# Kernel tuning notes

Measured on AMD Instinct MI355X. Metric: run time of the kernel, lower is better.

## Reference

```python
import jax, jax.numpy as jnp
import numpy as np

N, E = 50000, 800000
F_IN, F_OUT, H, F_EDGE = 256, 32, 8, 5
LEAKY_SLOPE = 0.2


def setup_inputs() -> dict:
    key = jax.random.key(0)
    ks = jax.random.split(key, 6)
    x = jax.random.normal(ks[0], (N, F_IN), dtype=jnp.float32)
    edge_index = jax.random.randint(ks[1], (2, E), 0, N, dtype=jnp.int64)
    edge_attr = jax.random.normal(ks[2], (E, F_EDGE), dtype=jnp.float32)
    degree_src = jax.random.randint(ks[3], (E,), 0, 64, dtype=jnp.int64)
    # Xavier-uniform params
    lim_W = float(np.sqrt(6.0 / (F_IN + F_OUT)))
    W = jax.random.uniform(ks[4], (H, F_IN, F_OUT), minval=-lim_W, maxval=lim_W, dtype=jnp.float32)
    A = 2 * F_OUT + F_EDGE
    lim_a = float(np.sqrt(6.0 / (H + A)))
    a = jax.random.uniform(ks[5], (H, A), minval=-lim_a, maxval=lim_a, dtype=jnp.float32)
    lim_e = float(np.sqrt(1.0 / F_EDGE))
    W_edge_w = jax.random.uniform(jax.random.fold_in(key, 7), (F_EDGE, F_EDGE), minval=-lim_e, maxval=lim_e, dtype=jnp.float32)
    return {"x": x, "edge_index": edge_index, "edge_attr": edge_attr,
            "degree_src": degree_src, "W": W, "a": a, "W_edge_w": W_edge_w}


def reference(x, edge_index, edge_attr, degree_src, W, a, W_edge_w):
    n = x.shape[0]
    h, f_out = W.shape[0], W.shape[2]
    src, dst = edge_index[0], edge_index[1]
    # per-head projection: (N, H, F_out)
    Wh = jnp.einsum('nf,hfo->nho', x, W)
    # split attention vector instead of materializing the concat
    a_src, a_dst, a_e = a[:, :f_out], a[:, f_out:2 * f_out], a[:, 2 * f_out:]
    ef = edge_attr @ W_edge_w.T                      # (E, F_edge)
    e = (jnp.einsum('eho,ho->eh', Wh[src], a_src)
         + jnp.einsum('eho,ho->eh', Wh[dst], a_dst)
         + ef @ a_e.T)                                # (E, H)
    e = jax.nn.leaky_relu(e, LEAKY_SLOPE)
    scale = 1.0 / jnp.sqrt(jnp.clip(degree_src.astype(jnp.float32), 1.0, None))
    e = e * scale[:, None]
    # segment softmax over src; torch scatter_reduce amax include_self=True with zeros init -> max includes 0
    e_max = jnp.maximum(jax.ops.segment_max(e, src, num_segments=n), 0.0)
    e_exp = jnp.exp(e - e_max[src])
    e_sum = jax.ops.segment_sum(e_exp, src, num_segments=n)
    alpha = e_exp / (e_sum[src] + 1e-16)             # (E, H)
    msg = Wh[dst] * alpha[:, :, None]                # (E, H, F_out)
    out = jax.ops.segment_sum(msg, src, num_segments=n)
    out = jax.nn.elu(out.reshape(n, h * f_out))
    return out, alpha
```

## Files before the change

### kernel.cpp

```cpp
#include <hip/hip_runtime.h>
#include <hip/hip_bf16.h>
#include <math.h>

#define NN 50000
#define NE 800000
#define FIN 256
#define FOUT 32
#define NH 8
#define FE 5
#define AROW 69
#define NROWS_PAD 50048
#define BSTRIDE 48

typedef float f32x4 __attribute__((ext_vector_type(4)));
typedef short bf16x8 __attribute__((ext_vector_type(8)));

static __device__ __forceinline__ unsigned short f2bf(float f) {
    unsigned u = __float_as_uint(f);
    unsigned r = (u + 0x7FFFu + ((u >> 16) & 1u)) >> 16;
    return (unsigned short)r;
}
static __device__ __forceinline__ float bf2f(unsigned short b) {
    return __uint_as_float(((unsigned)b) << 16);
}
static __device__ __forceinline__ short f2bf_fast(float f) {
    __hip_bfloat16 h = __float2bfloat16(f);
    return *reinterpret_cast<short*>(&h);
}

__global__ __launch_bounds__(256) void k_prepre(const float* __restrict__ W,
                                                const float* __restrict__ a,
                                                const float* __restrict__ Wew,
                                                const int* __restrict__ ei,
                                                float* __restrict__ C,
                                                unsigned short* __restrict__ Bh,
                                                unsigned short* __restrict__ Bsh,
                                                unsigned short* __restrict__ Bsl,
                                                int* __restrict__ counts,
                                                int* __restrict__ pos) {
    int b = blockIdx.x, t = threadIdx.x;
    int i = b * 256 + t;
    if (i < NE / 4) {
        int4 e4 = *(const int4*)&ei[i * 4];
        int4 pv;
        pv.x = atomicAdd(&counts[e4.x], 1);
        pv.y = atomicAdd(&counts[e4.y], 1);
        pv.z = atomicAdd(&counts[e4.z], 1);
        pv.w = atomicAdd(&counts[e4.w], 1);
        *(int4*)&pos[i * 4] = pv;
    }
    if (b < 256) {
        int c = b, k = t;
        int h = c >> 5, o = c & 31;
        Bh[c * 256 + k] = f2bf(W[(size_t)h * (FIN * FOUT) + (size_t)k * FOUT + o]);
    } else if (b == 256) {
        if (t < NH * FE) {
            int h = t / FE, k = t % FE;
            float s = 0.f;
            for (int j = 0; j < FE; ++j) s += a[h * AROW + 2 * FOUT + j] * Wew[j * FE + k];
            C[t] = s;
        }
        int k = t;
        for (int h = 0; h < NH; ++h) {
            float s1v = 0.f, s2v = 0.f;
            for (int o = 0; o < FOUT; ++o) {
                float wv = W[(size_t)h * (FIN * FOUT) + (size_t)k * FOUT + o];
                s1v += wv * a[h * AROW + o];
                s2v += wv * a[h * AROW + FOUT + o];
            }
            unsigned short h1 = f2bf(s1v);
            Bsh[h * 256 + k] = h1;
            Bsl[h * 256 + k] = f2bf(s1v - bf2f(h1));
            unsigned short h2 = f2bf(s2v);
            Bsh[(8 + h) * 256 + k] = h2;
            Bsl[(8 + h) * 256 + k] = f2bf(s2v - bf2f(h2));
        }
    }
}

__global__ __launch_bounds__(256) void k_gemm_mfma(const float* __restrict__ x,
                                                   const unsigned short* __restrict__ Bh,
                                                   const unsigned short* __restrict__ Bsh,
                                                   const unsigned short* __restrict__ Bsl,
                                                   unsigned short* __restrict__ Whb,
                                                   float* __restrict__ s1,
                                                   float* __restrict__ s2, int nrows) {
    int t = threadIdx.x;
    int w = t >> 6, l = t & 63;
    int r = l & 15, blk = l >> 4;
    int row0 = blockIdx.x * 32;
    int c0 = w * 64;

    f32x4 acc[2][4];
    f32x4 acc_s = (f32x4)(0.f);
#pragma unroll
    for (int i = 0; i < 2; ++i)
#pragma unroll
        for (int j = 0; j < 4; ++j) acc[i][j] = (f32x4)(0.f);

    const float* ap[2];
#pragma unroll
    for (int rt = 0; rt < 2; ++rt) {
        int row = row0 + rt * 16 + r;
        if (row >= nrows) row = nrows - 1;
        ap[rt] = x + (size_t)row * 256 + blk * 8;
    }

#pragma unroll
    for (int ks = 0; ks < 8; ++ks) {
        const int k0 = ks * 32;
        bf16x8 ah[2];
#pragma unroll
        for (int rt = 0; rt < 2; ++rt) {
            f32x4 u0 = *(const f32x4*)(ap[rt] + k0);
            f32x4 u1 = *(const f32x4*)(ap[rt] + k0 + 4);
            ah[rt][0] = f2bf_fast(u0.x); ah[rt][1] = f2bf_fast(u0.y);
            ah[rt][2] = f2bf_fast(u0.z); ah[rt][3] = f2bf_fast(u0.w);
            ah[rt][4] = f2bf_fast(u1.x); ah[rt][5] = f2bf_fast(u1.y);
            ah[rt][6] = f2bf_fast(u1.z); ah[rt][7] = f2bf_fast(u1.w);
        }
        bf16x8 bh[4];
#pragma unroll
        for (int ct = 0; ct < 4; ++ct) {
            int c = c0 + ct * 16 + r;
            bh[ct] = *(const bf16x8*)&Bh[c * 256 + k0 + blk * 8];
        }
#pragma unroll
        for (int ct = 0; ct < 4; ++ct) {
#pragma unroll
            for (int rt = 0; rt < 2; ++rt)
                acc[rt][ct] = __builtin_amdgcn_mfma_f32_16x16x32_bf16(ah[rt], bh[ct], acc[rt][ct], 0, 0, 0);
        }
        if (w < 2) {
            bf16x8 bsh = *(const bf16x8*)&Bsh[r * 256 + k0 + blk * 8];
            bf16x8 bsl = *(const bf16x8*)&Bsl[r * 256 + k0 + blk * 8];
            acc_s = __builtin_amdgcn_mfma_f32_16x16x32_bf16(ah[w], bsh, acc_s, 0, 0, 0);
            acc_s = __builtin_amdgcn_mfma_f32_16x16x32_bf16(ah[w], bsl, acc_s, 0, 0, 0);
        }
    }

#pragma unroll
    for (int rt = 0; rt < 2; ++rt) {
#pragma unroll
        for (int reg = 0; reg < 4; ++reg) {
            int row = row0 + rt * 16 + blk * 4 + reg;
            if (row < nrows) {
#pragma unroll
                for (int ct = 0; ct < 4; ++ct)
                    Whb[(size_t)row * 256 + c0 + ct * 16 + r] = f2bf(acc[rt][ct][reg]);
            }
        }
    }
    if (w < 2) {
#pragma unroll
        for (int reg = 0; reg < 4; ++reg) {
            int row = row0 + w * 16 + blk * 4 + reg;
            if (row < nrows) {
                if (r < 8) s1[row * NH + r] = acc_s[reg];
                else       s2[row * NH + (r - 8)] = acc_s[reg];
            }
        }
    }
}

__global__ __launch_bounds__(256) void k_scatlog(const int* __restrict__ ei,
                                                 const float* __restrict__ eattr,
                                                 const int* __restrict__ degs,
                                                 const float* __restrict__ s1,
                                                 const float* __restrict__ s2,
                                                 const float* __restrict__ C,
                                                 const int* __restrict__ pos,
                                                 unsigned short* __restrict__ e_perm,
                                                 int2* __restrict__ de_perm) {
    __shared__ float Cl[NH * FE];
    int t = threadIdx.x;
    if (t < NH * FE) Cl[t] = C[t];
    __syncthreads();
    int e = blockIdx.x * 256 + t;
    if (e >= NE) return;
    int src = ei[e], dst = ei[NE + e];
    int dg = degs[e];
    float scale = rsqrtf((float)(dg > 1 ? dg : 1));
    float ea0 = eattr[(size_t)e * FE + 0];
    float ea1 = eattr[(size_t)e * FE + 1];
    float ea2 = eattr[(size_t)e * FE + 2];
    float ea3 = eattr[(size_t)e * FE + 3];
    float ea4 = eattr[(size_t)e * FE + 4];
    float4 s1a = *(const float4*)&s1[src * NH];
    float4 s1b = *(const float4*)&s1[src * NH + 4];
    float4 s2a = *(const float4*)&s2[dst * NH];
    float4 s2b = *(const float4*)&s2[dst * NH + 4];
    float vs1[8] = {s1a.x, s1a.y, s1a.z, s1a.w, s1b.x, s1b.y, s1b.z, s1b.w};
    float vs2[8] = {s2a.x, s2a.y, s2a.z, s2a.w, s2b.x, s2b.y, s2b.z, s2b.w};
    bf16x8 v;
#pragma unroll
    for (int h = 0; h < NH; ++h) {
        float q = vs1[h] + vs2[h] + ea0 * Cl[h * FE + 0] + ea1 * Cl[h * FE + 1] +
                  ea2 * Cl[h * FE + 2] + ea3 * Cl[h * FE + 3] + ea4 * Cl[h * FE + 4];
        q = q > 0.f ? q : 0.2f * q;
        v[h] = (short)f2bf(q * scale);
    }
    int ps = pos[e];
    if (ps < BSTRIDE) {
        int p = src * BSTRIDE + ps;
        *(bf16x8*)&e_perm[(size_t)p * 8] = v;
        de_perm[p] = make_int2(dst, e);
    }
}

__global__ __launch_bounds__(256) void k_smmsg(const int* __restrict__ counts,
                                               const unsigned short* __restrict__ e_perm,
                                               const int2* __restrict__ de_perm,
                                               const unsigned short* __restrict__ Whb,
                                               float* __restrict__ out_alpha,
                                               float* __restrict__ out) {
    __shared__ float al[4][256];
    __shared__ int dl[4][32];
    __shared__ int el[4][32];
    int t = threadIdx.x;
    int w = t >> 6, l = t & 63;
    int n = blockIdx.x * 4 + w;
    if (n >= NN) return;
    int start = n * BSTRIDE;
    int deg = counts[n];
    if (deg > BSTRIDE) deg = BSTRIDE;
    int j = l >> 3, h = l & 7;

    float vc[4];
#pragma unroll
    for (int q = 0; q < 4; ++q) {
        int b = j + 8 * q;
        vc[q] = (b < deg) ? bf2f(e_perm[(size_t)(start + b) * 8 + h]) : -1e30f;
    }
    float mx = 0.f;
#pragma unroll
    for (int q = 0; q < 4; ++q) mx = fmaxf(mx, vc[q]);
    for (int b = 32 + j; b < deg; b += 8)
        mx = fmaxf(mx, bf2f(e_perm[(size_t)(start + b) * 8 + h]));
    mx = fmaxf(mx, __shfl_xor(mx, 8));
    mx = fmaxf(mx, __shfl_xor(mx, 16));
    mx = fmaxf(mx, __shfl_xor(mx, 32));
    float m = mx;
    float ex[4];
    float sm = 0.f;
#pragma unroll
    for (int q = 0; q < 4; ++q) { ex[q] = __expf(vc[q] - m); sm += ex[q]; }
    for (int b = 32 + j; b < deg; b += 8)
        sm += __expf(bf2f(e_perm[(size_t)(start + b) * 8 + h]) - m);
    sm += __shfl_xor(sm, 8);
    sm += __shfl_xor(sm, 16);
    sm += __shfl_xor(sm, 32);
    float inv = 1.f / (sm + 1e-16f);
    f32x4 acc = (f32x4)(0.f);
    int hh = l >> 3;
    for (int base = 0; base < deg; base += 32) {
        int cnt = deg - base;
        if (cnt > 32) cnt = 32;
        if (l < cnt) {
            int2 de = de_perm[start + base + l];
            dl[w][l] = de.x;
            el[w][l] = de.y;
        }
        asm volatile("s_waitcnt lgkmcnt(0)" ::: "memory");
#pragma unroll
        for (int q = 0; q < 4; ++q) {
            int b = base + j + 8 * q;
            if (b < deg) {
                float av = (base == 0 ? ex[q]
                                      : __expf(bf2f(e_perm[(size_t)(start + b) * 8 + h]) - m)) * inv;
                al[w][(j + 8 * q) * 8 + h] = av;
                out_alpha[(size_t)el[w][j + 8 * q] * 8 + h] = av;
            }
        }
        asm volatile("s_waitcnt lgkmcnt(0)" ::: "memory");
        int jj = 0;
        for (; jj + 4 <= cnt; jj += 4) {
            int d0 = dl[w][jj], d1 = dl[w][jj + 1], d2 = dl[w][jj + 2], d3 = dl[w][jj + 3];
            float a0 = al[w][jj * 8 + hh],      a1 = al[w][jj * 8 + 8 + hh];
            float a2 = al[w][jj * 8 + 16 + hh], a3 = al[w][jj * 8 + 24 + hh];
            ushort4 u0 = *(const ushort4*)&Whb[(size_t)d0 * 256 + l * 4];
            ushort4 u1 = *(const ushort4*)&Whb[(size_t)d1 * 256 + l * 4];
            ushort4 u2 = *(const ushort4*)&Whb[(size_t)d2 * 256 + l * 4];
            ushort4 u3 = *(const ushort4*)&Whb[(size_t)d3 * 256 + l * 4];
            acc.x += a0 * bf2f(u0.x) + a1 * bf2f(u1.x) + a2 * bf2f(u2.x) + a3 * bf2f(u3.x);
            acc.y += a0 * bf2f(u0.y) + a1 * bf2f(u1.y) + a2 * bf2f(u2.y) + a3 * bf2f(u3.y);
            acc.z += a0 * bf2f(u0.z) + a1 * bf2f(u1.z) + a2 * bf2f(u2.z) + a3 * bf2f(u3.z);
            acc.w += a0 * bf2f(u0.w) + a1 * bf2f(u1.w) + a2 * bf2f(u2.w) + a3 * bf2f(u3.w);
        }
        for (; jj < cnt; ++jj) {
            int d0 = dl[w][jj];
            float a0 = al[w][jj * 8 + hh];
            ushort4 u0 = *(const ushort4*)&Whb[(size_t)d0 * 256 + l * 4];
            acc.x += a0 * bf2f(u0.x);
            acc.y += a0 * bf2f(u0.y);
            acc.z += a0 * bf2f(u0.z);
            acc.w += a0 * bf2f(u0.w);
        }
        asm volatile("s_waitcnt lgkmcnt(0)" ::: "memory");
    }
    f32x4 o;
    o.x = acc.x > 0.f ? acc.x : expm1f(acc.x);
    o.y = acc.y > 0.f ? acc.y : expm1f(acc.y);
    o.z = acc.z > 0.f ? acc.z : expm1f(acc.z);
    o.w = acc.w > 0.f ? acc.w : expm1f(acc.w);
    *(f32x4*)&out[(size_t)n * 256 + l * 4] = o;
}

extern "C" void kernel_launch(void* const* d_in, const int* in_sizes, int n_in,
                              void* d_out, int out_size, void* d_ws, size_t ws_size,
                              hipStream_t stream) {
    const float* x     = (const float*)d_in[0];
    const int*   ei    = (const int*)d_in[1];
    const float* eattr = (const float*)d_in[2];
    const int*   degs  = (const int*)d_in[3];
    const float* W     = (const float*)d_in[4];
    const float* a     = (const float*)d_in[5];
    const float* Wew   = (const float*)d_in[6];

    float* out       = (float*)d_out;
    float* out_alpha = out + (size_t)NN * 256;

    char* p = (char*)d_ws;
    auto alloc = [&](size_t bytes) -> char* {
        char* r = p;
        p += (bytes + 255) & ~(size_t)255;
        return r;
    };
    unsigned short* Whb     = (unsigned short*)alloc((size_t)NN * 256 * 2);
    float*          s1      = (float*)alloc((size_t)NN * NH * 4);
    float*          s2      = (float*)alloc((size_t)NN * NH * 4);
    float*          Cm      = (float*)alloc(NH * FE * 4);
    unsigned short* Bh      = (unsigned short*)alloc((size_t)256 * 256 * 2);
    unsigned short* Bsh     = (unsigned short*)alloc((size_t)16 * 256 * 2);
    unsigned short* Bsl     = (unsigned short*)alloc((size_t)16 * 256 * 2);
    int*            counts  = (int*)alloc((size_t)NN * 4);
    int*            pos     = (int*)alloc((size_t)NE * 4);
    unsigned short* e_perm  = (unsigned short*)alloc(((size_t)NN * BSTRIDE + 64) * NH * 2);
    int2*           de_perm = (int2*)alloc(((size_t)NN * BSTRIDE + 64) * 8);

    hipMemsetAsync(counts, 0, (size_t)NN * 4, stream);

    k_prepre<<<(NE / 4 + 255) / 256, 256, 0, stream>>>(W, a, Wew, ei, Cm, Bh,
                                                       Bsh, Bsl, counts, pos);
    k_gemm_mfma<<<NROWS_PAD / 32, 256, 0, stream>>>(x, Bh, Bsh, Bsl, Whb, s1, s2, NN);
    k_scatlog<<<(NE + 255) / 256, 256, 0, stream>>>(ei, eattr, degs, s1, s2, Cm,
                                                    pos, e_perm, de_perm);
    k_smmsg<<<(NN + 3) / 4, 256, 0, stream>>>(counts, e_perm, de_perm, Whb,
                                              out_alpha, out);
}
```

Measured before the change: 223.1 us.

## Stage bf16 A tile in LDS and double GEMM row tile to 64

```diff
diff --git a/kernel.cpp b/kernel.cpp
--- a/kernel.cpp
+++ b/kernel.cpp
@@ -11,6 +11,7 @@
 #define AROW 69
 #define NROWS_PAD 50048
 #define BSTRIDE 48
+#define ASTRIDE 264
 
 typedef float f32x4 __attribute__((ext_vector_type(4)));
 typedef short bf16x8 __attribute__((ext_vector_type(8)));
@@ -85,53 +86,58 @@
                                                    unsigned short* __restrict__ Whb,
                                                    float* __restrict__ s1,
                                                    float* __restrict__ s2, int nrows) {
+    __shared__ __align__(16) unsigned short Ah[64 * ASTRIDE];
     int t = threadIdx.x;
     int w = t >> 6, l = t & 63;
     int r = l & 15, blk = l >> 4;
-    int row0 = blockIdx.x * 32;
+    int row0 = blockIdx.x * 64;
     int c0 = w * 64;
 
-    f32x4 acc[2][4];
+#pragma unroll
+    for (int i = 0; i < 16; ++i) {
+        int row = row0 + w * 16 + i;
+        if (row >= nrows) row = nrows - 1;
+        f32x4 u = *(const f32x4*)&x[(size_t)row * 256 + l * 4];
+        short b0 = f2bf_fast(u.x), b1 = f2bf_fast(u.y);
+        short b2 = f2bf_fast(u.z), b3 = f2bf_fast(u.w);
+        ushort4 pk;
+        pk.x = (unsigned short)b0; pk.y = (unsigned short)b1;
+        pk.z = (unsigned short)b2; pk.w = (unsigned short)b3;
+        *(ushort4*)&Ah[(w * 16 + i) * ASTRIDE + l * 4] = pk;
+    }
+    __syncthreads();
+
+    f32x4 acc[4][4];
     f32x4 acc_s = (f32x4)(0.f);
 #pragma unroll
-    for (int i = 0; i < 2; ++i)
+    for (int i = 0; i < 4; ++i)
 #pragma unroll
         for (int j = 0; j < 4; ++j) acc[i][j] = (f32x4)(0.f);
 
-    const float* ap[2];
-#pragma unroll
-    for (int rt = 0; rt < 2; ++rt) {
-        int row = row0 + rt * 16 + r;
-        if (row >= nrows) row = nrows - 1;
-        ap[rt] = x + (size_t)row * 256 + blk * 8;
-    }
+    const unsigned short* bp0 = &Bh[(c0 + 0 * 16 + r) * 256 + blk * 8];
+    const unsigned short* bp1 = &Bh[(c0 + 1 * 16 + r) * 256 + blk * 8];
+    const unsigned short* bp2 = &Bh[(c0 + 2 * 16 + r) * 256 + blk * 8];
+    const unsigned short* bp3 = &Bh[(c0 + 3 * 16 + r) * 256 + blk * 8];
 
 #pragma unroll
     for (int ks = 0; ks < 8; ++ks) {
         const int k0 = ks * 32;
-        bf16x8 ah[2];
-#pragma unroll
-        for (int rt = 0; rt < 2; ++rt) {
-            f32x4 u0 = *(const f32x4*)(ap[rt] + k0);
-            f32x4 u1 = *(const f32x4*)(ap[rt] + k0 + 4);
-            ah[rt][0] = f2bf_fast(u0.x); ah[rt][1] = f2bf_fast(u0.y);
-            ah[rt][2] = f2bf_fast(u0.z); ah[rt][3] = f2bf_fast(u0.w);
-            ah[rt][4] = f2bf_fast(u1.x); ah[rt][5] = f2bf_fast(u1.y);
-            ah[rt][6] = f2bf_fast(u1.z); ah[rt][7] = f2bf_fast(u1.w);
-        }
+        bf16x8 ah[4];
+#pragma unroll
+        for (int rt = 0; rt < 4; ++rt)
+            ah[rt] = *(const bf16x8*)&Ah[(rt * 16 + r) * ASTRIDE + k0 + blk * 8];
         bf16x8 bh[4];
+        bh[0] = *(const bf16x8*)(bp0 + k0);
+        bh[1] = *(const bf16x8*)(bp1 + k0);
+        bh[2] = *(const bf16x8*)(bp2 + k0);
+        bh[3] = *(const bf16x8*)(bp3 + k0);
 #pragma unroll
         for (int ct = 0; ct < 4; ++ct) {
-            int c = c0 + ct * 16 + r;
-            bh[ct] = *(const bf16x8*)&Bh[c * 256 + k0 + blk * 8];
-        }
-#pragma unroll
-        for (int ct = 0; ct < 4; ++ct) {
-#pragma unroll
-            for (int rt = 0; rt < 2; ++rt)
+#pragma unroll
+            for (int rt = 0; rt < 4; ++rt)
                 acc[rt][ct] = __builtin_amdgcn_mfma_f32_16x16x32_bf16(ah[rt], bh[ct], acc[rt][ct], 0, 0, 0);
         }
-        if (w < 2) {
+        {
             bf16x8 bsh = *(const bf16x8*)&Bsh[r * 256 + k0 + blk * 8];
             bf16x8 bsl = *(const bf16x8*)&Bsl[r * 256 + k0 + blk * 8];
             acc_s = __builtin_amdgcn_mfma_f32_16x16x32_bf16(ah[w], bsh, acc_s, 0, 0, 0);
@@ -140,7 +146,7 @@
     }
 
 #pragma unroll
-    for (int rt = 0; rt < 2; ++rt) {
+    for (int rt = 0; rt < 4; ++rt) {
 #pragma unroll
         for (int reg = 0; reg < 4; ++reg) {
             int row = row0 + rt * 16 + blk * 4 + reg;
@@ -151,14 +157,12 @@
             }
         }
     }
-    if (w < 2) {
-#pragma unroll
-        for (int reg = 0; reg < 4; ++reg) {
-            int row = row0 + w * 16 + blk * 4 + reg;
-            if (row < nrows) {
-                if (r < 8) s1[row * NH + r] = acc_s[reg];
-                else       s2[row * NH + (r - 8)] = acc_s[reg];
-            }
+#pragma unroll
+    for (int reg = 0; reg < 4; ++reg) {
+        int row = row0 + w * 16 + blk * 4 + reg;
+        if (row < nrows) {
+            if (r < 8) s1[row * NH + r] = acc_s[reg];
+            else       s2[row * NH + (r - 8)] = acc_s[reg];
         }
     }
 }
@@ -342,7 +346,7 @@
 
     k_prepre<<<(NE / 4 + 255) / 256, 256, 0, stream>>>(W, a, Wew, ei, Cm, Bh,
                                                        Bsh, Bsl, counts, pos);
-    k_gemm_mfma<<<NROWS_PAD / 32, 256, 0, stream>>>(x, Bh, Bsh, Bsl, Whb, s1, s2, NN);
+    k_gemm_mfma<<<NROWS_PAD / 64, 256, 0, stream>>>(x, Bh, Bsh, Bsl, Whb, s1, s2, NN);
     k_scatlog<<<(NE + 255) / 256, 256, 0, stream>>>(ei, eattr, degs, s1, s2, Cm,
                                                     pos, e_perm, de_perm);
     k_smmsg<<<(NN + 3) / 4, 256, 0, stream>>>(counts, e_perm, de_perm, Whb,
```

Result: no change. 223.7 us, median of 2 (+0.3%).
